# Optimization experiments

Measured on AMD Instinct MI355X. Metric: run time of the kernel, lower is better.

## Reference

```python
import jax, jax.numpy as jnp
import numpy as np

KS = 3      # kernel size
PAD = 1     # zero padding
STRIDE = 1
N = KS * KS # 9 sampling points per pixel


def _deform_conv(feature, offset, weight):
    """DeformConv2d: bilinear sample at learned offsets then 3x3 conv (no bias)."""
    b, c, h, w = feature.shape
    x = jnp.pad(feature, ((0, 0), (0, 0), (PAD, PAD), (PAD, PAD)))
    hp, wp = h + 2 * PAD, w + 2 * PAD
    dt = feature.dtype
    # p_n: kernel grid offsets, x(rows) first then y(cols) -> (2N,)
    rng = jnp.arange(-(KS - 1) // 2, (KS - 1) // 2 + 1, dtype=dt)
    pn_x, pn_y = jnp.meshgrid(rng, rng, indexing='ij')
    # p_0: base sampling grid starting at 1 (accounts for zero padding)
    p0_x, p0_y = jnp.meshgrid(jnp.arange(1, h + 1, dtype=dt),
                              jnp.arange(1, w + 1, dtype=dt), indexing='ij')
    # sampling locations p = p_0 + p_n + offset, split into x/y -> (b,h,w,N)
    off = jnp.transpose(offset, (0, 2, 3, 1))  # (b,h,w,2N)
    px = p0_x[None, :, :, None] + pn_x.reshape(-1)[None, None, None, :] + off[..., :N]
    py = p0_y[None, :, :, None] + pn_y.reshape(-1)[None, None, None, :] + off[..., N:]
    q_lt_x = jnp.clip(jnp.floor(px), 0, hp - 1)
    q_lt_y = jnp.clip(jnp.floor(py), 0, wp - 1)
    q_rb_x = jnp.clip(jnp.floor(px) + 1, 0, hp - 1)
    q_rb_y = jnp.clip(jnp.floor(py) + 1, 0, wp - 1)
    px = jnp.clip(px, 0, hp - 1)
    py = jnp.clip(py, 0, wp - 1)
    # bilinear weights for the 4 corners
    g_lt = (1 + (q_lt_x - px)) * (1 + (q_lt_y - py))
    g_rb = (1 - (q_rb_x - px)) * (1 - (q_rb_y - py))
    g_lb = (1 + (q_lt_x - px)) * (1 - (q_rb_y - py))
    g_rt = (1 - (q_rb_x - px)) * (1 + (q_lt_y - py))
    x_flat = x.reshape(b, c, hp * wp)

    def gather(qx, qy):
        idx = (qx * wp + qy).astype(jnp.int32).reshape(b, 1, -1)
        v = jnp.take_along_axis(x_flat, jnp.broadcast_to(idx, (b, c, h * w * N)), axis=2)
        return v.reshape(b, c, h, w, N)

    x_off = (g_lt[:, None] * gather(q_lt_x, q_lt_y)
             + g_rb[:, None] * gather(q_rb_x, q_rb_y)
             + g_lb[:, None] * gather(q_lt_x, q_rb_y)
             + g_rt[:, None] * gather(q_rb_x, q_lt_y))  # (b,c,h,w,N)
    # equivalent of _reshape_x_offset + conv(ks, stride=ks)
    x_off = x_off.reshape(b, c, h, w, KS, KS)
    return jnp.einsum('bchwij,ocij->bohw', x_off, weight)


def setup_inputs() -> dict:
    key = jax.random.key(0)
    k1, k2, k3 = jax.random.split(key, 3)
    B, C, H, W = 4, 256, 64, 64
    feature = jax.random.normal(k1, (B, C, H, W), dtype=jnp.float32)
    offset = jax.random.normal(k2, (B, 2 * N, H, W), dtype=jnp.float32)
    weight = jax.random.normal(k3, (C, C, KS, KS), dtype=jnp.float32) / np.sqrt(C * N)
    return {"feature": feature, "offset": offset, "weight": weight}


def reference(feature, offset, weight):
    f1 = jax.nn.relu(_deform_conv(feature, offset, weight))
    return jax.nn.relu(f1 + feature)
```

## Files before the change

### kernel.cpp

```cpp
#include <hip/hip_runtime.h>

#define HW    4096
#define J_TOT 16384
#define K_TOT 2304
#define C_CH  256

typedef unsigned short u16;
typedef unsigned int   u32;
typedef __attribute__((ext_vector_type(8))) short short8;
typedef __attribute__((ext_vector_type(4))) float f32x4;
typedef __attribute__((ext_vector_type(8))) unsigned short us8;

__device__ __forceinline__ float b2f(u16 u) { return __uint_as_float(((u32)u) << 16); }
__device__ __forceinline__ u16 f2b(float x) {
  u32 u = __float_as_uint(x);
  u += 0x7FFFu + ((u >> 16) & 1u);
  return (u16)(u >> 16);
}

__device__ __forceinline__ void gload_lds16(const u16* g, u16* l) {
  __builtin_amdgcn_global_load_lds(
      (__attribute__((address_space(1))) void*)(void*)g,
      (__attribute__((address_space(3))) void*)(void*)l, 16, 0, 0);
}

__global__ void k_detect(const u16* __restrict__ f, int* __restrict__ flag) {
  __shared__ int sh[256];
  int t = threadIdx.x;
  int hits = 0;
  for (int i = t; i < 2048; i += 256) {
    u16 u = f[2 * i];
    int e = (u >> 7) & 0xFF;
    hits += (e >= 100 && e <= 141) ? 1 : 0;
  }
  sh[t] = hits;
  __syncthreads();
  if (t == 0) {
    int s = 0;
    for (int i = 0; i < 256; i++) s += sh[i];
    flag[0] = (s > 1024) ? 1 : 0;
  }
}

__global__ void k_transpose(const void* __restrict__ featv, u16* __restrict__ ftr,
                            const int* __restrict__ flag) {
  __shared__ u16 tile[32][33];
  int isbf = *flag;
  int b = blockIdx.z;
  int hw0 = blockIdx.x << 5;
  int c0 = blockIdx.y << 5;
  int tx = threadIdx.x;
  int ty = threadIdx.y;
  if (isbf) {
    const u16* f = (const u16*)featv;
#pragma unroll
    for (int i = 0; i < 4; i++) {
      int c = c0 + ty + i * 8;
      tile[ty + i * 8][tx] = f[(((size_t)(b * C_CH + c)) << 12) + hw0 + tx];
    }
  } else {
    const float* f = (const float*)featv;
#pragma unroll
    for (int i = 0; i < 4; i++) {
      int c = c0 + ty + i * 8;
      tile[ty + i * 8][tx] = f2b(f[(((size_t)(b * C_CH + c)) << 12) + hw0 + tx]);
    }
  }
  __syncthreads();
#pragma unroll
  for (int i = 0; i < 4; i++) {
    int hw = hw0 + ty + i * 8;
    ftr[(((size_t)(b * HW + hw)) << 8) + c0 + tx] = tile[tx][ty + i * 8];
  }
}

__global__ void k_wconv(const void* __restrict__ wv, u16* __restrict__ Wr,
                        const int* __restrict__ flag) {
  int isbf = *flag;
  int idx = blockIdx.x * 256 + threadIdx.x;
  if (idx >= C_CH * K_TOT) return;
  int c = idx & 255;
  int n = (idx >> 8) % 9;
  int o = idx / K_TOT;
  int src = (o * 256 + c) * 9 + n;
  if (isbf) Wr[idx] = ((const u16*)wv)[src];
  else      Wr[idx] = f2b(((const float*)wv)[src]);
}

__global__ __launch_bounds__(256) void k_gather(const void* __restrict__ offv,
                                                const u16* __restrict__ ftr,
                                                u16* __restrict__ Xt,
                                                const int* __restrict__ flag) {
  __shared__ float gs[9][4][16];
  __shared__ int   isx[9][4][16];
  int isbf = *flag;
  int j0 = blockIdx.x << 4;
  int b = j0 >> 12;
  int hw0 = j0 & (HW - 1);
  int t = threadIdx.x;

  if (t < 144) {
    int p = t & 15, n = t >> 4;
    int hw = hw0 + p;
    int h = hw >> 6, w = hw & 63;
    size_t obi = (((size_t)(b * 18 + n)) << 12) + hw;
    float ox, oy;
    if (isbf) {
      const u16* po = (const u16*)offv;
      ox = b2f(po[obi]);
      oy = b2f(po[obi + (9u << 12)]);
    } else {
      const float* po = (const float*)offv;
      ox = po[obi];
      oy = po[obi + (9u << 12)];
    }
    int ki = n / 3, kj = n % 3;
    float px = (float)(h + ki) + ox;
    float py = (float)(w + kj) + oy;
    float fx = floorf(px), fy = floorf(py);
    float qltx = fminf(fmaxf(fx, 0.f), 65.f);
    float qlty = fminf(fmaxf(fy, 0.f), 65.f);
    float qrbx = fminf(fmaxf(fx + 1.f, 0.f), 65.f);
    float qrby = fminf(fmaxf(fy + 1.f, 0.f), 65.f);
    float pcx = fminf(fmaxf(px, 0.f), 65.f);
    float pcy = fminf(fmaxf(py, 0.f), 65.f);
    float dltx = 1.f + (qltx - pcx);
    float drbx = 1.f - (qrbx - pcx);
    float dlty = 1.f + (qlty - pcy);
    float drby = 1.f - (qrby - pcy);
    float g0 = dltx * dlty;
    float g1 = drbx * drby;
    float g2 = dltx * drby;
    float g3 = drbx * dlty;
    int x0 = (int)qltx, y0 = (int)qlty, x1 = (int)qrbx, y1 = (int)qrby;
    int v0 = (x0 >= 1 && x0 <= 64 && y0 >= 1 && y0 <= 64);
    int v1 = (x1 >= 1 && x1 <= 64 && y1 >= 1 && y1 <= 64);
    int v2 = (x0 >= 1 && x0 <= 64 && y1 >= 1 && y1 <= 64);
    int v3 = (x1 >= 1 && x1 <= 64 && y0 >= 1 && y0 <= 64);
    int base = b << 12;
    isx[n][0][p] = v0 ? ((base + ((x0 - 1) << 6) + (y0 - 1)) << 8) : 0;
    isx[n][1][p] = v1 ? ((base + ((x1 - 1) << 6) + (y1 - 1)) << 8) : 0;
    isx[n][2][p] = v2 ? ((base + ((x0 - 1) << 6) + (y1 - 1)) << 8) : 0;
    isx[n][3][p] = v3 ? ((base + ((x1 - 1) << 6) + (y0 - 1)) << 8) : 0;
    gs[n][0][p] = v0 ? g0 : 0.f;
    gs[n][1][p] = v1 ? g1 : 0.f;
    gs[n][2][p] = v2 ? g2 : 0.f;
    gs[n][3][p] = v3 ? g3 : 0.f;
  }
  __syncthreads();

  int p = t >> 4, cq = t & 15;
  size_t rowb = (size_t)(j0 + p) * K_TOT;
  int cA = cq * 8, cB = 128 + cq * 8;
  for (int n = 0; n < 9; n++) {
    float g0 = gs[n][0][p], g1 = gs[n][1][p], g2 = gs[n][2][p], g3 = gs[n][3][p];
    const u16* f0 = ftr + isx[n][0][p];
    const u16* f1 = ftr + isx[n][1][p];
    const u16* f2 = ftr + isx[n][2][p];
    const u16* f3 = ftr + isx[n][3][p];
    u16* dst = Xt + rowb + n * 256;
#pragma unroll
    for (int half = 0; half < 2; half++) {
      int c = half ? cB : cA;
      us8 r0 = *(const us8*)(f0 + c);
      us8 r1 = *(const us8*)(f1 + c);
      us8 r2 = *(const us8*)(f2 + c);
      us8 r3 = *(const us8*)(f3 + c);
      us8 ov;
#pragma unroll
      for (int i = 0; i < 8; i++) {
        float v = g0 * b2f(r0[i]) + g1 * b2f(r1[i]) + g2 * b2f(r2[i]) + g3 * b2f(r3[i]);
        ov[i] = f2b(v);
      }
      *(us8*)(dst + c) = ov;
    }
  }
}

__global__ __launch_bounds__(256) void k_gemm(const u16* __restrict__ Wr,
                                              const u16* __restrict__ Xt,
                                              const void* __restrict__ featv,
                                              void* __restrict__ outv,
                                              const int* __restrict__ flag) {
  __shared__ u16 Bs[128 * 32];
  __shared__ u16 As[64 * 32];
  int isbf = *flag;
  int jb = blockIdx.x << 7;
  int ob0 = blockIdx.y << 6;
  int t = threadIdx.x;
  int wave = t >> 6, lane = t & 63;
  int wj = wave >> 1, wo = wave & 1;
  int lr = lane & 15, lk = lane >> 4;

  f32x4 acc[2][4];
  f32x4 zero = {0.f, 0.f, 0.f, 0.f};
#pragma unroll
  for (int i = 0; i < 2; i++)
#pragma unroll
    for (int j = 0; j < 4; j++) acc[i][j] = zero;

  int s0 = wave * 64 + lane;
  int s1 = 256 + s0;
  int r0 = s0 >> 2, cg0 = (s0 & 3) ^ ((r0 >> 1) & 3);
  int r1 = s1 >> 2, cg1 = (s1 & 3) ^ ((r1 >> 1) & 3);
  const u16* bg0 = Xt + (size_t)(jb + r0) * K_TOT + cg0 * 8;
  const u16* bg1 = Xt + (size_t)(jb + r1) * K_TOT + cg1 * 8;
  const u16* ag  = Wr + (size_t)(ob0 + r0) * K_TOT + cg0 * 8;
  u16* bl0 = &Bs[wave * 512];
  u16* bl1 = &Bs[2048 + wave * 512];
  u16* al  = &As[wave * 512];

  int swz = (lr >> 1) & 3;
  const u16* ar = &As[(wo * 32 + lr) * 32 + (lk ^ swz) * 8];
  const u16* br = &Bs[(wj * 64 + lr) * 32 + (lk ^ swz) * 8];

  for (int k0 = 0; k0 < K_TOT; k0 += 32) {
    gload_lds16(bg0 + k0, bl0);
    gload_lds16(bg1 + k0, bl1);
    gload_lds16(ag + k0, al);
    __syncthreads();
    short8 a[2], bb[4];
#pragma unroll
    for (int oi = 0; oi < 2; oi++) a[oi] = *(const short8*)(ar + oi * 512);
#pragma unroll
    for (int ji = 0; ji < 4; ji++) bb[ji] = *(const short8*)(br + ji * 512);
#pragma unroll
    for (int oi = 0; oi < 2; oi++)
#pragma unroll
      for (int ji = 0; ji < 4; ji++)
        acc[oi][ji] = __builtin_amdgcn_mfma_f32_16x16x32_bf16(a[oi], bb[ji], acc[oi][ji], 0, 0, 0);
    __syncthreads();
  }

  int lq = lane >> 4;
#pragma unroll
  for (int oi = 0; oi < 2; oi++) {
#pragma unroll
    for (int ji = 0; ji < 4; ji++) {
      int j = jb + wj * 64 + ji * 16 + lr;
      int bb_ = j >> 12, hw = j & (HW - 1);
      int o0 = ob0 + wo * 32 + oi * 16 + lq * 4;
#pragma unroll
      for (int r = 0; r < 4; r++) {
        size_t oidx = (((size_t)(bb_ * C_CH + o0 + r)) << 12) + hw;
        float v = acc[oi][ji][r];
        v = fmaxf(v, 0.f);
        float ft = isbf ? b2f(((const u16*)featv)[oidx]) : ((const float*)featv)[oidx];
        v = fmaxf(v + ft, 0.f);
        if (isbf) ((u16*)outv)[oidx] = f2b(v);
        else      ((float*)outv)[oidx] = v;
      }
    }
  }
}

extern "C" void kernel_launch(void* const* d_in, const int* in_sizes, int n_in,
                              void* d_out, int out_size, void* d_ws, size_t ws_size,
                              hipStream_t stream) {
  const void* feat = d_in[0];
  const void* offs = d_in[1];
  const void* wght = d_in[2];

  const size_t off_flag = 0;
  const size_t off_wr   = 256;
  const size_t off_ftr  = off_wr + (size_t)1179648;
  const size_t off_xt   = off_ftr + (size_t)8388608;
  const size_t need     = off_xt + (size_t)75497472;
  if (ws_size < need) return;

  char* ws = (char*)d_ws;
  int* flag = (int*)(ws + off_flag);
  u16* Wr   = (u16*)(ws + off_wr);
  u16* ftr  = (u16*)(ws + off_ftr);
  u16* Xt   = (u16*)(ws + off_xt);

  k_detect<<<1, 256, 0, stream>>>((const u16*)feat, flag);
  k_transpose<<<dim3(128, 8, 4), dim3(32, 8), 0, stream>>>(feat, ftr, flag);
  k_wconv<<<K_TOT, 256, 0, stream>>>(wght, Wr, flag);
  k_gather<<<J_TOT / 16, 256, 0, stream>>>(offs, ftr, Xt, flag);
  k_gemm<<<dim3(J_TOT / 128, 4), 256, 0, stream>>>(Wr, Xt, feat, d_out, flag);
}
```

Baseline: 142.6 us.

## Triple-buffer GEMM LDS tiles with K=64 stages and async prefetch

Reworks the GEMM main loop to use three LDS buffers holding K=64 tiles. Global-to-LDS loads for stage t+2 are issued while stage t is computed, with a vmcnt wait and a single barrier per iteration in place of two syncthreads. It also changes the XOR swizzle to suit 64-wide rows and raises wave priority around the MFMA block. The aim is to hide global load latency and halve barrier overhead, at the cost of more LDS (72KB), which may lower occupancy.

```diff
diff --git a/kernel.cpp b/kernel.cpp
--- a/kernel.cpp
+++ b/kernel.cpp
@@ -177,20 +177,63 @@
   }
 }
 
+#define NT 36
+
+#define GEMM_STAGE(bufi)                                                     \
+  do {                                                                       \
+    u16* _bl = &Bs[bufi][wave * 2048];                                       \
+    u16* _al = &As[bufi][wave * 1024];                                       \
+    gload_lds16(bsrc0, _bl);                                                 \
+    gload_lds16(bsrc1, _bl + 512);                                           \
+    gload_lds16(bsrc2, _bl + 1024);                                          \
+    gload_lds16(bsrc3, _bl + 1536);                                          \
+    gload_lds16(asrc0, _al);                                                 \
+    gload_lds16(asrc1, _al + 512);                                           \
+    bsrc0 += 64; bsrc1 += 64; bsrc2 += 64; bsrc3 += 64;                      \
+    asrc0 += 64; asrc1 += 64;                                                \
+  } while (0)
+
+#define GEMM_COMPUTE(bufi)                                                   \
+  do {                                                                       \
+    short8 af[2][2], bf[4][2];                                               \
+    _Pragma("unroll")                                                        \
+    for (int kk = 0; kk < 2; kk++) {                                         \
+      int go = (((kk << 2) + lk) ^ swz) << 3;                                \
+      _Pragma("unroll")                                                      \
+      for (int oi = 0; oi < 2; oi++)                                         \
+        af[oi][kk] = *(const short8*)(As[bufi] + (wo * 32 + oi * 16 + lr) * 64 + go); \
+      _Pragma("unroll")                                                      \
+      for (int ji = 0; ji < 4; ji++)                                         \
+        bf[ji][kk] = *(const short8*)(Bs[bufi] + (wj * 64 + ji * 16 + lr) * 64 + go); \
+    }                                                                        \
+    __builtin_amdgcn_s_setprio(1);                                           \
+    _Pragma("unroll")                                                        \
+    for (int kk = 0; kk < 2; kk++)                                           \
+      _Pragma("unroll")                                                      \
+      for (int oi = 0; oi < 2; oi++)                                         \
+        _Pragma("unroll")                                                    \
+        for (int ji = 0; ji < 4; ji++)                                       \
+          acc[oi][ji] = __builtin_amdgcn_mfma_f32_16x16x32_bf16(             \
+              af[oi][kk], bf[ji][kk], acc[oi][ji], 0, 0, 0);                 \
+    __builtin_amdgcn_s_setprio(0);                                           \
+  } while (0)
+
 __global__ __launch_bounds__(256) void k_gemm(const u16* __restrict__ Wr,
                                               const u16* __restrict__ Xt,
                                               const void* __restrict__ featv,
                                               void* __restrict__ outv,
                                               const int* __restrict__ flag) {
-  __shared__ u16 Bs[128 * 32];
-  __shared__ u16 As[64 * 32];
+  __shared__ u16 Bs[3][128 * 64];
+  __shared__ u16 As[3][64 * 64];
   int isbf = *flag;
+  asm volatile("" :: "s"(isbf));
   int jb = blockIdx.x << 7;
   int ob0 = blockIdx.y << 6;
   int t = threadIdx.x;
   int wave = t >> 6, lane = t & 63;
   int wj = wave >> 1, wo = wave & 1;
   int lr = lane & 15, lk = lane >> 4;
+  int swz = lr & 7;
 
   f32x4 acc[2][4];
   f32x4 zero = {0.f, 0.f, 0.f, 0.f};
@@ -199,38 +242,34 @@
 #pragma unroll
     for (int j = 0; j < 4; j++) acc[i][j] = zero;
 
-  int s0 = wave * 64 + lane;
-  int s1 = 256 + s0;
-  int r0 = s0 >> 2, cg0 = (s0 & 3) ^ ((r0 >> 1) & 3);
-  int r1 = s1 >> 2, cg1 = (s1 & 3) ^ ((r1 >> 1) & 3);
-  const u16* bg0 = Xt + (size_t)(jb + r0) * K_TOT + cg0 * 8;
-  const u16* bg1 = Xt + (size_t)(jb + r1) * K_TOT + cg1 * 8;
-  const u16* ag  = Wr + (size_t)(ob0 + r0) * K_TOT + cg0 * 8;
-  u16* bl0 = &Bs[wave * 512];
-  u16* bl1 = &Bs[2048 + wave * 512];
-  u16* al  = &As[wave * 512];
-
-  int swz = (lr >> 1) & 3;
-  const u16* ar = &As[(wo * 32 + lr) * 32 + (lk ^ swz) * 8];
-  const u16* br = &Bs[(wj * 64 + lr) * 32 + (lk ^ swz) * 8];
-
-  for (int k0 = 0; k0 < K_TOT; k0 += 32) {
-    gload_lds16(bg0 + k0, bl0);
-    gload_lds16(bg1 + k0, bl1);
-    gload_lds16(ag + k0, al);
-    __syncthreads();
-    short8 a[2], bb[4];
-#pragma unroll
-    for (int oi = 0; oi < 2; oi++) a[oi] = *(const short8*)(ar + oi * 512);
-#pragma unroll
-    for (int ji = 0; ji < 4; ji++) bb[ji] = *(const short8*)(br + ji * 512);
-#pragma unroll
-    for (int oi = 0; oi < 2; oi++)
-#pragma unroll
-      for (int ji = 0; ji < 4; ji++)
-        acc[oi][ji] = __builtin_amdgcn_mfma_f32_16x16x32_bf16(a[oi], bb[ji], acc[oi][ji], 0, 0, 0);
-    __syncthreads();
-  }
+  int rb = lane >> 3;
+  int cs = ((lane & 7) ^ rb) << 3;
+  const u16* bsrc0 = Xt + (size_t)(jb + wave * 32 +  0 + rb) * K_TOT + cs;
+  const u16* bsrc1 = Xt + (size_t)(jb + wave * 32 +  8 + rb) * K_TOT + cs;
+  const u16* bsrc2 = Xt + (size_t)(jb + wave * 32 + 16 + rb) * K_TOT + cs;
+  const u16* bsrc3 = Xt + (size_t)(jb + wave * 32 + 24 + rb) * K_TOT + cs;
+  const u16* asrc0 = Wr + (size_t)(ob0 + wave * 16 + 0 + rb) * K_TOT + cs;
+  const u16* asrc1 = Wr + (size_t)(ob0 + wave * 16 + 8 + rb) * K_TOT + cs;
+
+  GEMM_STAGE(0);
+  GEMM_STAGE(1);
+  asm volatile("s_waitcnt vmcnt(6)" ::: "memory");
+  __builtin_amdgcn_s_barrier();
+
+  int cb = 0, sb = 2;
+  for (int tt = 0; tt < NT - 2; ++tt) {
+    GEMM_STAGE(sb);
+    GEMM_COMPUTE(cb);
+    asm volatile("s_waitcnt vmcnt(6)" ::: "memory");
+    __builtin_amdgcn_s_barrier();
+    cb = (cb + 1 == 3) ? 0 : cb + 1;
+    sb = (sb + 1 == 3) ? 0 : sb + 1;
+  }
+  GEMM_COMPUTE(cb);
+  asm volatile("s_waitcnt vmcnt(0)" ::: "memory");
+  __builtin_amdgcn_s_barrier();
+  cb = (cb + 1 == 3) ? 0 : cb + 1;
+  GEMM_COMPUTE(cb);
 
   int lq = lane >> 4;
 #pragma unroll
```

After: 140.7 us. No clear change (-1.3%).
